# Kernel tuning notes

Measured on AMD Instinct MI355X. Metric: run time of the kernel, lower is better.

Reference implementation:

```python
import jax, jax.numpy as jnp
import numpy as np

A = 9               # anchors per location (3 scales x 3 ratios)
STRIDE = 32         # backbone stride 16 * conv1 stride 2
PRE_NMS = 2000      # boxes kept before NMS
POST_NMS = 300      # rois kept after NMS
NMS_THRESH = 0.7
MIN_SIZE = 16.0
NEG = jnp.float32(-1e30)


def _generate_anchors(base_size=16, ratios=(0.5, 1.0, 2.0), scales=(8, 16, 32)):
    xc = yc = 0.5 * (base_size - 1)
    size = float(base_size * base_size)
    anchors = []
    for r in ratios:
        ws = np.round(np.sqrt(size / r))
        hs = np.round(ws * r)
        for s in scales:
            w, h = ws * s, hs * s
            anchors.append([xc - 0.5 * (w - 1), yc - 0.5 * (h - 1),
                            xc + 0.5 * (w - 1), yc + 0.5 * (h - 1)])
    return np.array(anchors, dtype=np.float32)  # [A,4]


def _conv(x, w, b, stride, pad):
    y = jax.lax.conv_general_dilated(
        x, w, (stride, stride), ((pad, pad), (pad, pad)),
        dimension_numbers=('NCHW', 'OIHW', 'NCHW'))
    return y + b[None, :, None, None]


def _iou_matrix(boxes):
    x1, y1, x2, y2 = boxes[:, 0], boxes[:, 1], boxes[:, 2], boxes[:, 3]
    area = (x2 - x1 + 1.0) * (y2 - y1 + 1.0)
    iw = jnp.maximum(0.0, jnp.minimum(x2[:, None], x2[None, :]) - jnp.maximum(x1[:, None], x1[None, :]) + 1.0)
    ih = jnp.maximum(0.0, jnp.minimum(y2[:, None], y2[None, :]) - jnp.maximum(y1[:, None], y1[None, :]) + 1.0)
    inter = iw * ih
    return inter / (area[:, None] + area[None, :] - inter)


def _nms_single(boxes, scores):
    # boxes [K,4] sorted by score desc; scores [K] (NEG = filtered out)
    K = boxes.shape[0]
    iou = _iou_matrix(boxes)
    prio = jnp.arange(K, 0, -1)

    def step(valid, _):
        any_valid = jnp.any(valid)
        pick = jnp.argmax(jnp.where(valid, prio, 0))
        new_valid = valid & (iou[pick] <= NMS_THRESH)
        return new_valid, (pick, any_valid)

    valid0 = scores > NEG * 0.5
    _, (picks, flags) = jax.lax.scan(step, valid0, None, length=POST_NMS)
    sel = boxes[picks] * flags[:, None].astype(boxes.dtype)
    return sel, jnp.sum(flags.astype(jnp.int32))


def _proposal(deltas, scores):
    B, _, H, W = deltas.shape
    im_h, im_w = float(H * STRIDE), float(W * STRIDE)
    anchors = jnp.asarray(_generate_anchors())  # [A,4]
    sx = (jnp.arange(W) * STRIDE).astype(jnp.float32)
    sy = (jnp.arange(H) * STRIDE).astype(jnp.float32)
    gx, gy = jnp.meshgrid(sx, sy)  # [H,W] each
    shift = jnp.stack([gx, gy, gx, gy], axis=-1)  # [H,W,4]
    anc = (shift[:, :, None, :] + anchors[None, None, :, :]).reshape(-1, 4)  # [H*W*A,4]

    d = deltas.reshape(B, A, 4, H, W).transpose(0, 3, 4, 1, 2).reshape(B, -1, 4)  # [B,N,4]
    s = scores[:, A:].transpose(0, 2, 3, 1).reshape(B, -1)  # fg scores [B,N]

    ws = anc[:, 2] - anc[:, 0] + 1.0
    hs = anc[:, 3] - anc[:, 1] + 1.0
    cx = anc[:, 0] + 0.5 * ws
    cy = anc[:, 1] + 0.5 * hs
    pcx = d[:, :, 0] * ws + cx
    pcy = d[:, :, 1] * hs + cy
    pw = jnp.exp(d[:, :, 2]) * ws
    ph = jnp.exp(d[:, :, 3]) * hs
    boxes = jnp.stack([pcx - 0.5 * pw, pcy - 0.5 * ph,
                       pcx + 0.5 * pw, pcy + 0.5 * ph], axis=-1)  # [B,N,4]
    lim = jnp.array([im_w - 1, im_h - 1, im_w - 1, im_h - 1], jnp.float32)
    boxes = jnp.minimum(jnp.maximum(boxes, 0.0), lim)

    bw = boxes[..., 2] - boxes[..., 0] + 1.0
    bh = boxes[..., 3] - boxes[..., 1] + 1.0
    s = jnp.where((bw >= MIN_SIZE) & (bh >= MIN_SIZE), s, NEG)

    top_s, idx = jax.lax.top_k(s, PRE_NMS)  # sorted desc
    top_b = jnp.take_along_axis(boxes, idx[:, :, None], axis=1)  # [B,PRE,4]

    sel, num = jax.vmap(_nms_single)(top_b, top_s)  # [B,POST,4], [B]
    bidx = jnp.broadcast_to(jnp.arange(B, dtype=sel.dtype)[:, None, None], (B, POST_NMS, 1))
    rois = jnp.concatenate([bidx, sel], axis=-1)  # [B,POST,5]
    return rois, num


def setup_inputs() -> dict:
    key = jax.random.key(0)
    k = jax.random.split(key, 4)
    x = jax.random.normal(k[0], (4, 512, 96, 160), jnp.float32)
    w1 = jax.random.normal(k[1], (512, 512, 3, 3), jnp.float32) * 0.02
    b1 = jnp.zeros((512,), jnp.float32)
    w_bbox = jax.random.normal(k[2], (36, 512, 1, 1), jnp.float32) * 0.02
    b_bbox = jnp.zeros((36,), jnp.float32)
    w_cls = jax.random.normal(k[3], (18, 512, 3, 3), jnp.float32) * 0.02
    b_cls = jnp.zeros((18,), jnp.float32)
    return dict(x=x, w1=w1, b1=b1, w_bbox=w_bbox, b_bbox=b_bbox, w_cls=w_cls, b_cls=b_cls)


def reference(x, w1, b1, w_bbox, b_bbox, w_cls, b_cls):
    feat = _conv(x, w1, b1, 2, 1)           # [B,512,H/2,W/2]
    deltas = _conv(feat, w_bbox, b_bbox, 1, 0)  # [B,36,h,w]
    cls = _conv(feat, w_cls, b_cls, 1, 1)       # [B,18,h,w]
    return _proposal(deltas, cls)
```

## Files before the change

kernel.cpp:

```cpp
#include <hip/hip_runtime.h>
#include <stdint.h>

typedef unsigned long long u64;
typedef unsigned int u32;

__constant__ float c_aw[9] = {184.f,368.f,736.f,128.f,256.f,512.f, 88.f,176.f,352.f};
__constant__ float c_ah[9] = { 96.f,192.f,384.f,128.f,256.f,512.f,176.f,352.f,704.f};

__global__ __launch_bounds__(256) void transpose_k(const float* __restrict__ w1,
                                                   float* __restrict__ wt2) {
  int e = blockIdx.x * 256 + threadIdx.x;
  int m = e & 7;
  int t = e >> 3;
  int k = t % 9;
  int r = t / 9;
  int ci = r & 511;
  int g = r >> 9;
  wt2[e] = w1[(size_t)(g * 8 + m) * 4608 + ci * 9 + k];
}

__global__ __launch_bounds__(256, 3) void conv1_k(const float* __restrict__ x,
                                                  const float* __restrict__ wt2,
                                                  const float* __restrict__ b1,
                                                  float* __restrict__ feat) {
  __shared__ float xs[8 * 9 * 164];
  const int tid = threadIdx.x;
  const int lane = tid & 63;
  const int wv = __builtin_amdgcn_readfirstlane(tid >> 6);
  const int owg = lane & 15;
  const int ohl = lane >> 4;
  const int n = blockIdx.z;
  const int gg = blockIdx.x * 4 + wv;
  const int oh0 = blockIdx.y * 4;
  const int ih_base = 2 * oh0 - 1;

  int soff[6], loff[6];
  float okf[6];
  bool act[6];
#pragma unroll
  for (int it = 0; it < 6; ++it) {
    int e2 = tid + 256 * it;
    act[it] = (e2 < 1449);
    int e = act[it] ? e2 : 0;
    int ih = e / 161;
    int c = e - ih * 161;
    int gih = ih_base + ih;
    int giw = c - 1;
    bool ok = act[it] && ((unsigned)gih < 96u) && ((unsigned)giw < 160u);
    soff[it] = min(max(gih, 0), 95) * 160 + min(max(giw, 0), 159);
    loff[it] = ih * 164 + c;
    okf[it] = ok ? 1.f : 0.f;
  }

  float acc[8][5];
#pragma unroll
  for (int m = 0; m < 8; ++m)
#pragma unroll
    for (int j = 0; j < 5; ++j) acc[m][j] = 0.f;

  const float* xb = x + (size_t)n * 512 * 96 * 160;
  const float* wgb = wt2 + (size_t)gg * 512 * 72;

  float r[6][8];
#pragma unroll
  for (int it = 0; it < 6; ++it)
#pragma unroll
    for (int ci = 0; ci < 8; ++ci)
      r[it][ci] = xb[(size_t)ci * 15360 + soff[it]];

  for (int c0 = 0; c0 < 512; c0 += 8) {
    __syncthreads();
#pragma unroll
    for (int it = 0; it < 6; ++it) {
      if (act[it]) {
        const float m_ = okf[it];
#pragma unroll
        for (int ci = 0; ci < 8; ++ci)
          xs[loff[it] + ci * 1476] = m_ * r[it][ci];
      }
    }
    __syncthreads();
    if (c0 + 8 < 512) {
      const float* xn = xb + (size_t)(c0 + 8) * 15360;
#pragma unroll
      for (int it = 0; it < 6; ++it)
#pragma unroll
        for (int ci = 0; ci < 8; ++ci)
          r[it][ci] = xn[(size_t)ci * 15360 + soff[it]];
    }

    for (int ci = 0; ci < 8; ++ci) {
      const float* wp = wgb + (size_t)(c0 + ci) * 72;
      const float* xrow = &xs[(ci * 9 + 2 * ohl) * 164 + owg * 10];
#pragma unroll
      for (int kh = 0; kh < 3; ++kh) {
        float xv[12];
        const float* xr = xrow + kh * 164;
#pragma unroll
        for (int t2 = 0; t2 < 6; ++t2) {
          float2 tt = *(const float2*)(xr + 2 * t2);
          xv[2 * t2] = tt.x; xv[2 * t2 + 1] = tt.y;
        }
#pragma unroll
        for (int kw = 0; kw < 3; ++kw) {
          const float* wk = wp + (kh * 3 + kw) * 8;
#pragma unroll
          for (int j = 0; j < 5; ++j) {
            const float xj = xv[kw + 2 * j];
            acc[0][j] += wk[0] * xj; acc[1][j] += wk[1] * xj;
            acc[2][j] += wk[2] * xj; acc[3][j] += wk[3] * xj;
            acc[4][j] += wk[4] * xj; acc[5][j] += wk[5] * xj;
            acc[6][j] += wk[6] * xj; acc[7][j] += wk[7] * xj;
          }
        }
      }
    }
  }
  const int oh = oh0 + ohl;
  const int owb = owg * 5;
#pragma unroll
  for (int m = 0; m < 8; ++m) {
    const int co = gg * 8 + m;
    const float bv = b1[co];
    float* op = &feat[(((size_t)n * 512 + co) * 48 + oh) * 80 + owb];
#pragma unroll
    for (int j = 0; j < 5; ++j) op[j] = acc[m][j] + bv;
  }
}

__global__ __launch_bounds__(256) void heads_k(const float* __restrict__ feat,
                                               const float* __restrict__ wb,
                                               const float* __restrict__ bb,
                                               const float* __restrict__ wcg,
                                               const float* __restrict__ bc,
                                               float* __restrict__ deltas,
                                               float* __restrict__ s) {
  __shared__ float smem[5328];
  const int tid = threadIdx.x;

  if (blockIdx.x < 120) {
    float* fs  = smem;
    float* wsb = smem + 2048;
    const int blk = blockIdx.x;
    const int b = blk / 30;
    const int pos0 = (blk % 30) * 128;
    const int pl = tid >> 1, cg = tid & 1;
    const int cbase = cg * 18;
    float acc[18];
#pragma unroll
    for (int j = 0; j < 18; ++j) acc[j] = 0.f;
    const float* fb = feat + (size_t)b * 512 * 3840;

    for (int c0 = 0; c0 < 512; c0 += 16) {
      for (int e = tid; e < 16 * 128; e += 256)
        fs[e] = fb[(size_t)(c0 + (e >> 7)) * 3840 + pos0 + (e & 127)];
      for (int e = tid; e < 16 * 36; e += 256) {
        int ci = e / 36, c = e - ci * 36;
        wsb[e] = wb[(size_t)c * 512 + c0 + ci];
      }
      __syncthreads();
      for (int ci = 0; ci < 16; ++ci) {
        float xv = fs[ci * 128 + pl];
#pragma unroll
        for (int j = 0; j < 18; ++j) acc[j] += xv * wsb[ci * 36 + cbase + j];
      }
      __syncthreads();
    }
    size_t o = ((size_t)b * 3840 + pos0 + pl) * 36 + cbase;
#pragma unroll
    for (int j = 0; j < 18; ++j) deltas[o + j] = acc[j] + bb[cbase + j];
  } else {
    float (*fs)[3][84] = (float(*)[3][84])smem;
    float (*wc)[9][9]  = (float(*)[9][9])(smem + 4032);
    const int bid2 = blockIdx.x - 120;
    const int oh = bid2 % 48;
    const int b = bid2 / 48;
    const int pos = tid % 80;
    const int cg = tid / 80;
    float acc[3] = {0.f, 0.f, 0.f};
    const float* fb = feat + (size_t)b * 512 * 3840;

    for (int c0 = 0; c0 < 512; c0 += 16) {
      for (int e = tid; e < 16 * 246; e += 256) {
        int ci = e / 246;
        int r = e - ci * 246;
        int ihl = r / 82;
        int iw = r - ihl * 82 - 1;
        int gih = oh - 1 + ihl;
        float v = 0.f;
        if ((unsigned)gih < 48u && (unsigned)iw < 80u)
          v = fb[(size_t)(c0 + ci) * 3840 + gih * 80 + iw];
        fs[ci][ihl][iw + 1] = v;
      }
      for (int e = tid; e < 16 * 81; e += 256) {
        int ci = e / 81;
        int r = e - ci * 81;
        int co = r / 9;
        int k = r - co * 9;
        wc[ci][co][k] = wcg[((size_t)(9 + co) * 512 + c0 + ci) * 9 + k];
      }
      __syncthreads();
      if (cg < 3) {
        const int cb = cg * 3;
        for (int ci = 0; ci < 16; ++ci) {
#pragma unroll
          for (int kh = 0; kh < 3; ++kh) {
#pragma unroll
            for (int kw = 0; kw < 3; ++kw) {
              float xv = fs[ci][kh][pos + kw];
              acc[0] += xv * wc[ci][cb + 0][kh * 3 + kw];
              acc[1] += xv * wc[ci][cb + 1][kh * 3 + kw];
              acc[2] += xv * wc[ci][cb + 2][kh * 3 + kw];
            }
          }
        }
      }
      __syncthreads();
    }
    if (cg < 3) {
      const int cb = cg * 3;
      size_t o = (size_t)b * 34560 + ((size_t)oh * 80 + pos) * 9 + cb;
#pragma unroll
      for (int j = 0; j < 3; ++j) s[o + j] = acc[j] + bc[9 + cb + j];
    }
  }
}

__global__ __launch_bounds__(256) void decode_k(const float* __restrict__ deltas,
                                                const float* __restrict__ s,
                                                float* __restrict__ boxes,
                                                u64* __restrict__ keys) {
  const int g = blockIdx.x * 256 + threadIdx.x;
  const int b = g / 34560;
  const int i = g - b * 34560;
  const int pos = i / 9;
  const int a = i - pos * 9;
  const int h = pos / 80;
  const int w = pos - h * 80;
  const float gx = (float)(w * 32);
  const float gy = (float)(h * 32);
  const float aw = c_aw[a], ah = c_ah[a];
  const float x1a = 7.5f - 0.5f * (aw - 1.f);
  const float y1a = 7.5f - 0.5f * (ah - 1.f);
  const float ws_ = aw, hs_ = ah;
  const float cx = (gx + x1a) + 0.5f * ws_;
  const float cy = (gy + y1a) + 0.5f * hs_;

  const float* dp = &deltas[((size_t)b * 3840 + pos) * 36 + a * 4];
  const float d0 = dp[0], d1 = dp[1], d2 = dp[2], d3 = dp[3];
  const float pcx = __fadd_rn(__fmul_rn(d0, ws_), cx);
  const float pcy = __fadd_rn(__fmul_rn(d1, hs_), cy);
  const float pw = __fmul_rn(expf(d2), ws_);
  const float ph = __fmul_rn(expf(d3), hs_);
  float bx1 = __fsub_rn(pcx, __fmul_rn(0.5f, pw));
  float by1 = __fsub_rn(pcy, __fmul_rn(0.5f, ph));
  float bx2 = __fadd_rn(pcx, __fmul_rn(0.5f, pw));
  float by2 = __fadd_rn(pcy, __fmul_rn(0.5f, ph));
  bx1 = fminf(fmaxf(bx1, 0.f), 2559.f);
  by1 = fminf(fmaxf(by1, 0.f), 1535.f);
  bx2 = fminf(fmaxf(bx2, 0.f), 2559.f);
  by2 = fminf(fmaxf(by2, 0.f), 1535.f);
  const float bw = __fadd_rn(__fsub_rn(bx2, bx1), 1.f);
  const float bh = __fadd_rn(__fsub_rn(by2, by1), 1.f);
  float sc = s[g];
  if (!(bw >= 16.f && bh >= 16.f)) sc = -1e30f;

  float4 bo;
  bo.x = bx1; bo.y = by1; bo.z = bx2; bo.w = by2;
  *(float4*)&boxes[(size_t)g * 4] = bo;

  u32 sb = __float_as_uint(sc);
  u32 ou = (sb & 0x80000000u) ? ~sb : (sb | 0x80000000u);
  keys[g] = ((u64)ou << 32) | (u32)(~(u32)i);
}

__global__ __launch_bounds__(1024) void selcomp_k(const u64* __restrict__ keys,
                                                  u64* __restrict__ sel) {
  __shared__ u32 h[16384];
  __shared__ u64 cand[6144];
  __shared__ u32 wsum[16], wsuf[16];
  __shared__ int s_bin, s_above, s_main, s_nc;
  const int b = blockIdx.x;
  const int tid = threadIdx.x;
  const int lane = tid & 63;
  const int wv = tid >> 6;
  const u64* kb = keys + (size_t)b * 34560;

#pragma unroll
  for (int q = 0; q < 16; ++q) h[tid + 1024 * q] = 0;
  __syncthreads();
  for (int i = tid; i < 34560; i += 1024)
    atomicAdd(&h[(u32)(kb[i] >> 50)], 1u);
  __syncthreads();

  const int i0 = tid * 16;
  u32 myb[16];
  u32 tsum = 0;
#pragma unroll
  for (int q = 0; q < 16; ++q) { myb[q] = h[i0 + q]; tsum += myb[q]; }
  u32 sfx = tsum;
#pragma unroll
  for (int off = 1; off < 64; off <<= 1) {
    u32 o = __shfl_down(sfx, off, 64);
    if (lane + off < 64) sfx += o;
  }
  if (lane == 0) wsum[wv] = sfx;
  __syncthreads();
  if (tid < 16) {
    u32 v = wsum[tid];
#pragma unroll
    for (int off = 1; off < 16; off <<= 1) {
      u32 o = __shfl_down(v, off, 64);
      if (tid + off < 16) v += o;
    }
    wsuf[tid] = v;
  }
  __syncthreads();
  const u32 wave_base = (wv < 15) ? wsuf[wv + 1] : 0u;
  u32 accu = wave_base + (sfx - tsum);
#pragma unroll
  for (int q = 15; q >= 0; --q) { accu += myb[q]; h[i0 + q] = accu; }
  __syncthreads();

#pragma unroll
  for (int q = 0; q < 16; ++q) {
    int bn = i0 + q;
    u32 Si = h[bn];
    u32 Sn = (bn < 16383) ? h[bn + 1] : 0u;
    if ((int)Si >= 2000 && (int)Sn < 2000) { s_bin = bn; s_above = (int)Sn; }
  }
  if (tid == 0) { s_main = 0; s_nc = 0; }
  __syncthreads();
  const u32 B = (u32)s_bin;
  const int above = s_above;
  const int need = 2000 - above;

  for (int i = tid; i < 34560; i += 1024) {
    u64 k = kb[i];
    u32 t14 = (u32)(k >> 50);
    if (t14 > B) {
      int p = atomicAdd(&s_main, 1);
      sel[(size_t)b * 2048 + p] = k;
    } else if (t14 == B) {
      int p = atomicAdd(&s_nc, 1);
      if (p < 6144) cand[p] = k;
    }
  }
  __syncthreads();
  const int nc = min(s_nc, 6144);
  for (int c = tid; c < nc; c += 1024) {
    u64 kc = cand[c];
    int rnk = 0;
    for (int j = 0; j < nc; ++j) rnk += (cand[j] > kc) ? 1 : 0;
    if (rnk < need) sel[(size_t)b * 2048 + above + rnk] = kc;
  }
}

__global__ __launch_bounds__(1024) void sort_k(const u64* __restrict__ sel,
                                               const float* __restrict__ boxes,
                                               float* __restrict__ sx1, float* __restrict__ sy1,
                                               float* __restrict__ sx2, float* __restrict__ sy2,
                                               float* __restrict__ sar, u32* __restrict__ sval) {
  __shared__ u64 K[2048];
  __shared__ unsigned char val[2048];
  const int b = blockIdx.x;
  const int tid = threadIdx.x;

  for (int i = tid; i < 2048; i += 1024)
    K[i] = (i < 2000) ? sel[(size_t)b * 2048 + i] : 0ull;
  __syncthreads();
  for (int k2 = 2; k2 <= 2048; k2 <<= 1) {
    for (int j = k2 >> 1; j > 0; j >>= 1) {
      for (int i = tid; i < 2048; i += 1024) {
        int l = i ^ j;
        if (l > i) {
          u64 a = K[i], c = K[l];
          bool up = ((i & k2) == 0);
          if (up ? (a < c) : (a > c)) { K[i] = c; K[l] = a; }
        }
      }
      __syncthreads();
    }
  }
  for (int i = tid; i < 2048; i += 1024) {
    float x1v = 0.f, y1v = 0.f, x2v = 0.f, y2v = 0.f, arv = 1.f;
    unsigned char vb = 0;
    if (i < 2000) {
      u64 key = K[i];
      u32 ou = (u32)(key >> 32);
      int idx = (int)(~(u32)key);
      u32 sb = (ou & 0x80000000u) ? (ou & 0x7FFFFFFFu) : ~ou;
      float sc = __uint_as_float(sb);
      const float4 bo = *(const float4*)&boxes[((size_t)b * 34560 + idx) * 4];
      x1v = bo.x; y1v = bo.y; x2v = bo.z; y2v = bo.w;
      arv = __fmul_rn(__fadd_rn(__fsub_rn(bo.z, bo.x), 1.f),
                      __fadd_rn(__fsub_rn(bo.w, bo.y), 1.f));
      vb = (sc > -5e29f) ? 1 : 0;
    }
    size_t o = (size_t)b * 2048 + i;
    sx1[o] = x1v; sy1[o] = y1v; sx2[o] = x2v; sy2[o] = y2v; sar[o] = arv;
    val[i] = vb;
  }
  __syncthreads();
  if (tid < 64) {
    u32 w = 0;
#pragma unroll
    for (int q = 0; q < 32; ++q)
      w |= (val[tid * 32 + q] ? 1u : 0u) << q;
    sval[b * 64 + tid] = w;
  }
}

__global__ __launch_bounds__(256) void iou_k(const float* __restrict__ sx1, const float* __restrict__ sy1,
                                             const float* __restrict__ sx2, const float* __restrict__ sy2,
                                             const float* __restrict__ sar,
                                             u64* __restrict__ supp) {
  __shared__ float lx1[2048], ly1[2048], lx2[2048], ly2[2048], lar[2048];
  const int b = blockIdx.y;
  const int r0 = blockIdx.x * 128;
  const int tid = threadIdx.x;
  const int lane = tid & 63;
  const int wq = tid >> 6;
  const size_t base = (size_t)b * 2048;

  for (int i = tid; i < 2048; i += 256) {
    lx1[i] = sx1[base + i]; ly1[i] = sy1[base + i];
    lx2[i] = sx2[base + i]; ly2[i] = sy2[base + i];
    lar[i] = sar[base + i];
  }
  __syncthreads();

  for (int i = r0; i < r0 + 128; ++i) {
    const float px1 = lx1[i], py1 = ly1[i], px2 = lx2[i], py2 = ly2[i], pa = lar[i];
    u64* row = supp + ((size_t)b * 2048 + i) * 32;
#pragma unroll
    for (int s2 = 0; s2 < 8; ++s2) {
      const int j = s2 * 256 + wq * 64 + lane;
      float iw = __fadd_rn(__fsub_rn(fminf(px2, lx2[j]), fmaxf(px1, lx1[j])), 1.f);
      iw = fmaxf(0.f, iw);
      float ih = __fadd_rn(__fsub_rn(fminf(py2, ly2[j]), fmaxf(py1, ly1[j])), 1.f);
      ih = fmaxf(0.f, ih);
      const float inter = __fmul_rn(iw, ih);
      const float denom = __fsub_rn(__fadd_rn(pa, lar[j]), inter);
      const float iou = __fdiv_rn(inter, denom);
      const u64 bits = __ballot(iou > 0.7f);
      if (lane == 0) row[s2 * 4 + wq] = bits;
    }
  }
}

__global__ __launch_bounds__(64) void scan_k(const u32* __restrict__ sval,
                                             const u64* __restrict__ supp,
                                             const float* __restrict__ sx1, const float* __restrict__ sy1,
                                             const float* __restrict__ sx2, const float* __restrict__ sy2,
                                             float* __restrict__ out) {
  const int b = blockIdx.x;
  const int lane = threadIdx.x;
  u32 v = sval[b * 64 + lane];
  const size_t base = (size_t)b * 2048;

  int cnt = 0;
  for (int t = 0; t < 300; ++t) {
    u64 m = __ballot(v != 0);
    if (m == 0) break;
    const int f = __ffsll(m) - 1;
    const u32 fw = __shfl(v, f, 64);
    const int p = f * 32 + (__ffs(fw) - 1);
    if (lane == 0) {
      float* row = out + ((size_t)b * 300 + t) * 5;
      row[0] = (float)b;
      row[1] = sx1[base + p]; row[2] = sy1[base + p];
      row[3] = sx2[base + p]; row[4] = sy2[base + p];
    }
    cnt = t + 1;
    const u64 w8 = supp[(base + p) * 32 + (lane >> 1)];
    const u32 sup = (lane & 1) ? (u32)(w8 >> 32) : (u32)w8;
    v &= ~sup;
  }
  for (int t2 = cnt + lane; t2 < 300; t2 += 64) {
    float* row = out + ((size_t)b * 300 + t2) * 5;
    row[0] = (float)b; row[1] = 0.f; row[2] = 0.f; row[3] = 0.f; row[4] = 0.f;
  }
  if (lane == 0) out[6000 + b] = (float)cnt;
}

extern "C" void kernel_launch(void* const* d_in, const int* in_sizes, int n_in,
                              void* d_out, int out_size, void* d_ws, size_t ws_size,
                              hipStream_t stream) {
  const float* x  = (const float*)d_in[0];
  const float* w1 = (const float*)d_in[1];
  const float* b1 = (const float*)d_in[2];
  const float* wb = (const float*)d_in[3];
  const float* bb = (const float*)d_in[4];
  const float* wc = (const float*)d_in[5];
  const float* bc = (const float*)d_in[6];
  float* out = (float*)d_out;
  char* ws = (char*)d_ws;

  float* feat   = (float*)(ws + 0);
  float* wt2    = (float*)(ws + 31457280);
  float* deltas = (float*)(ws + 40894464);
  float* s      = (float*)(ws + 43106304);
  float* boxes  = (float*)(ws + 43659264);
  u64*   keys   = (u64*)  (ws + 45871104);
  u64*   sel    = (u64*)  (ws + 46977088);
  float* sx1    = (float*)(ws + 47042624);
  float* sy1    = (float*)(ws + 47075392);
  float* sx2    = (float*)(ws + 47108160);
  float* sy2    = (float*)(ws + 47140928);
  float* sar    = (float*)(ws + 47173696);
  u32*   sval   = (u32*)  (ws + 47206464);
  u64*   supp   = (u64*)  (ws + 47207488);

  hipLaunchKernelGGL(transpose_k, dim3(9216), dim3(256), 0, stream, w1, wt2);
  hipLaunchKernelGGL(conv1_k, dim3(16, 12, 4), dim3(256), 0, stream, x, wt2, b1, feat);
  hipLaunchKernelGGL(heads_k, dim3(312), dim3(256), 0, stream, feat, wb, bb, wc, bc, deltas, s);
  hipLaunchKernelGGL(decode_k, dim3(540), dim3(256), 0, stream, deltas, s, boxes, keys);
  hipLaunchKernelGGL(selcomp_k, dim3(4), dim3(1024), 0, stream, keys, sel);
  hipLaunchKernelGGL(sort_k, dim3(4), dim3(1024), 0, stream, sel, boxes, sx1, sy1, sx2, sy2, sar, sval);
  hipLaunchKernelGGL(iou_k, dim3(16, 4), dim3(256), 0, stream, sx1, sy1, sx2, sy2, sar, supp);
  hipLaunchKernelGGL(scan_k, dim3(4), dim3(64), 0, stream, sval, supp, sx1, sy1, sx2, sy2, out);
}
```

Before: 1.544 ms.

## Pack conv1 FMAs into v2f and register-prefetch tiles in head kernels

The conv1 accumulators become float2 vectors so pairs of output channels share a packed FMA (v_pk_fma_f32 on CDNA), which halves the FMA instruction count in the hot inner loop. Both branches of the heads kernel switch from direct global-to-LDS staging to a register prefetch: the next 16-channel tile is loaded into registers while the current tile is computed, and one barrier per iteration is removed. This raises register pressure and depends on the compiler actually emitting the packed instructions.

Result: faster. 1.378 ms (-10.7%).

```diff
diff --git a/kernel.cpp b/kernel.cpp
--- a/kernel.cpp
+++ b/kernel.cpp
@@ -3,6 +3,7 @@
 
 typedef unsigned long long u64;
 typedef unsigned int u32;
+typedef float v2f __attribute__((ext_vector_type(2)));
 
 __constant__ float c_aw[9] = {184.f,368.f,736.f,128.f,256.f,512.f, 88.f,176.f,352.f};
 __constant__ float c_ah[9] = { 96.f,192.f,384.f,128.f,256.f,512.f,176.f,352.f,704.f};
@@ -52,11 +53,11 @@
     okf[it] = ok ? 1.f : 0.f;
   }
 
-  float acc[8][5];
-#pragma unroll
-  for (int m = 0; m < 8; ++m)
-#pragma unroll
-    for (int j = 0; j < 5; ++j) acc[m][j] = 0.f;
+  v2f acc[4][5];
+#pragma unroll
+  for (int q = 0; q < 4; ++q)
+#pragma unroll
+    for (int j = 0; j < 5; ++j) acc[q][j] = (v2f){0.f, 0.f};
 
   const float* xb = x + (size_t)n * 512 * 96 * 160;
   const float* wgb = wt2 + (size_t)gg * 512 * 72;
@@ -103,14 +104,16 @@
         }
 #pragma unroll
         for (int kw = 0; kw < 3; ++kw) {
-          const float* wk = wp + (kh * 3 + kw) * 8;
+          const v2f* wk2 = (const v2f*)(wp + (kh * 3 + kw) * 8);
+          const v2f w0 = wk2[0], w1 = wk2[1], w2 = wk2[2], w3 = wk2[3];
 #pragma unroll
           for (int j = 0; j < 5; ++j) {
             const float xj = xv[kw + 2 * j];
-            acc[0][j] += wk[0] * xj; acc[1][j] += wk[1] * xj;
-            acc[2][j] += wk[2] * xj; acc[3][j] += wk[3] * xj;
-            acc[4][j] += wk[4] * xj; acc[5][j] += wk[5] * xj;
-            acc[6][j] += wk[6] * xj; acc[7][j] += wk[7] * xj;
+            const v2f xx = {xj, xj};
+            acc[0][j] = __builtin_elementwise_fma(w0, xx, acc[0][j]);
+            acc[1][j] = __builtin_elementwise_fma(w1, xx, acc[1][j]);
+            acc[2][j] = __builtin_elementwise_fma(w2, xx, acc[2][j]);
+            acc[3][j] = __builtin_elementwise_fma(w3, xx, acc[3][j]);
           }
         }
       }
@@ -119,12 +122,16 @@
   const int oh = oh0 + ohl;
   const int owb = owg * 5;
 #pragma unroll
-  for (int m = 0; m < 8; ++m) {
-    const int co = gg * 8 + m;
-    const float bv = b1[co];
-    float* op = &feat[(((size_t)n * 512 + co) * 48 + oh) * 80 + owb];
-#pragma unroll
-    for (int j = 0; j < 5; ++j) op[j] = acc[m][j] + bv;
+  for (int q = 0; q < 4; ++q) {
+    const int co = gg * 8 + 2 * q;
+    const float bx = b1[co], by = b1[co + 1];
+    float* opx = &feat[(((size_t)n * 512 + co) * 48 + oh) * 80 + owb];
+    float* opy = opx + 3840;
+#pragma unroll
+    for (int j = 0; j < 5; ++j) {
+      opx[j] = acc[q][j].x + bx;
+      opy[j] = acc[q][j].y + by;
+    }
   }
 }
 
@@ -146,60 +153,122 @@
     const int pos0 = (blk % 30) * 128;
     const int pl = tid >> 1, cg = tid & 1;
     const int cbase = cg * 18;
+    const float* fb = feat + (size_t)b * 512 * 3840;
+
+    int fso[8];
+#pragma unroll
+    for (int p = 0; p < 8; ++p) {
+      int e = tid + 256 * p;
+      fso[p] = (e >> 7) * 3840 + pos0 + (e & 127);
+    }
+    int wso[3]; bool wact[3];
+#pragma unroll
+    for (int p = 0; p < 3; ++p) {
+      int e = tid + 256 * p;
+      wact[p] = (e < 576);
+      int ee = wact[p] ? e : 0;
+      wso[p] = (ee % 36) * 512 + (ee / 36);
+    }
     float acc[18];
 #pragma unroll
     for (int j = 0; j < 18; ++j) acc[j] = 0.f;
-    const float* fb = feat + (size_t)b * 512 * 3840;
-
-    for (int c0 = 0; c0 < 512; c0 += 16) {
-      for (int e = tid; e < 16 * 128; e += 256)
-        fs[e] = fb[(size_t)(c0 + (e >> 7)) * 3840 + pos0 + (e & 127)];
-      for (int e = tid; e < 16 * 36; e += 256) {
-        int ci = e / 36, c = e - ci * 36;
-        wsb[e] = wb[(size_t)c * 512 + c0 + ci];
-      }
+
+    float rf[8], rw[3];
+#pragma unroll
+    for (int p = 0; p < 8; ++p) rf[p] = fb[fso[p]];
+#pragma unroll
+    for (int p = 0; p < 3; ++p) rw[p] = wb[wso[p]];
+
+    for (int t = 0; t < 32; ++t) {
       __syncthreads();
+#pragma unroll
+      for (int p = 0; p < 8; ++p) fs[tid + 256 * p] = rf[p];
+#pragma unroll
+      for (int p = 0; p < 3; ++p)
+        if (wact[p]) wsb[tid + 256 * p] = rw[p];
+      __syncthreads();
+      if (t < 31) {
+        const float* fn = fb + (size_t)(t + 1) * 16 * 3840;
+        const float* wn = wb + (t + 1) * 16;
+#pragma unroll
+        for (int p = 0; p < 8; ++p) rf[p] = fn[fso[p]];
+#pragma unroll
+        for (int p = 0; p < 3; ++p) rw[p] = wn[wso[p]];
+      }
       for (int ci = 0; ci < 16; ++ci) {
         float xv = fs[ci * 128 + pl];
 #pragma unroll
         for (int j = 0; j < 18; ++j) acc[j] += xv * wsb[ci * 36 + cbase + j];
       }
-      __syncthreads();
     }
     size_t o = ((size_t)b * 3840 + pos0 + pl) * 36 + cbase;
 #pragma unroll
     for (int j = 0; j < 18; ++j) deltas[o + j] = acc[j] + bb[cbase + j];
   } else {
-    float (*fs)[3][84] = (float(*)[3][84])smem;
-    float (*wc)[9][9]  = (float(*)[9][9])(smem + 4032);
+    float* fsf = smem;
+    float* wcf = smem + 4032;
     const int bid2 = blockIdx.x - 120;
     const int oh = bid2 % 48;
     const int b = bid2 / 48;
     const int pos = tid % 80;
     const int cg = tid / 80;
+    const float* fb = feat + (size_t)b * 512 * 3840;
+
+    int fso3[16], lof3[16];
+    float fok3[16];
+    bool fact3[16];
+#pragma unroll
+    for (int p = 0; p < 16; ++p) {
+      int e = tid + 256 * p;
+      fact3[p] = (e < 3936);
+      int ee = fact3[p] ? e : 0;
+      int ci = ee / 246;
+      int r = ee - ci * 246;
+      int ihl = r / 82;
+      int iw = r - ihl * 82 - 1;
+      int gih = oh - 1 + ihl;
+      bool ok = fact3[p] && ((unsigned)gih < 48u) && ((unsigned)iw < 80u);
+      fso3[p] = ci * 3840 + min(max(gih, 0), 47) * 80 + min(max(iw, 0), 79);
+      lof3[p] = ci * 252 + ihl * 84 + iw + 1;
+      fok3[p] = ok ? 1.f : 0.f;
+    }
+    int wso3[6]; bool wact3[6];
+#pragma unroll
+    for (int p = 0; p < 6; ++p) {
+      int e = tid + 256 * p;
+      wact3[p] = (e < 1296);
+      int ee = wact3[p] ? e : 0;
+      int ci = ee / 81;
+      int r = ee - ci * 81;
+      int co = r / 9;
+      int k = r - co * 9;
+      wso3[p] = ((size_t)(9 + co) * 512 + ci) * 9 + k;
+    }
     float acc[3] = {0.f, 0.f, 0.f};
-    const float* fb = feat + (size_t)b * 512 * 3840;
-
-    for (int c0 = 0; c0 < 512; c0 += 16) {
-      for (int e = tid; e < 16 * 246; e += 256) {
-        int ci = e / 246;
-        int r = e - ci * 246;
-        int ihl = r / 82;
-        int iw = r - ihl * 82 - 1;
-        int gih = oh - 1 + ihl;
-        float v = 0.f;
-        if ((unsigned)gih < 48u && (unsigned)iw < 80u)
-          v = fb[(size_t)(c0 + ci) * 3840 + gih * 80 + iw];
-        fs[ci][ihl][iw + 1] = v;
-      }
-      for (int e = tid; e < 16 * 81; e += 256) {
-        int ci = e / 81;
-        int r = e - ci * 81;
-        int co = r / 9;
-        int k = r - co * 9;
-        wc[ci][co][k] = wcg[((size_t)(9 + co) * 512 + c0 + ci) * 9 + k];
-      }
+
+    float rf3[16], rw3[6];
+#pragma unroll
+    for (int p = 0; p < 16; ++p) rf3[p] = fb[fso3[p]];
+#pragma unroll
+    for (int p = 0; p < 6; ++p) rw3[p] = wcg[wso3[p]];
+
+    for (int t = 0; t < 32; ++t) {
       __syncthreads();
+#pragma unroll
+      for (int p = 0; p < 16; ++p)
+        if (fact3[p]) fsf[lof3[p]] = fok3[p] * rf3[p];
+#pragma unroll
+      for (int p = 0; p < 6; ++p)
+        if (wact3[p]) wcf[tid + 256 * p] = rw3[p];
+      __syncthreads();
+      if (t < 31) {
+        const float* fn = fb + (size_t)(t + 1) * 16 * 3840;
+        const float* wn = wcg + (t + 1) * 144;
+#pragma unroll
+        for (int p = 0; p < 16; ++p) rf3[p] = fn[fso3[p]];
+#pragma unroll
+        for (int p = 0; p < 6; ++p) rw3[p] = wn[wso3[p]];
+      }
       if (cg < 3) {
         const int cb = cg * 3;
         for (int ci = 0; ci < 16; ++ci) {
@@ -207,15 +276,14 @@
           for (int kh = 0; kh < 3; ++kh) {
 #pragma unroll
             for (int kw = 0; kw < 3; ++kw) {
-              float xv = fs[ci][kh][pos + kw];
-              acc[0] += xv * wc[ci][cb + 0][kh * 3 + kw];
-              acc[1] += xv * wc[ci][cb + 1][kh * 3 + kw];
-              acc[2] += xv * wc[ci][cb + 2][kh * 3 + kw];
+              float xv = fsf[ci * 252 + kh * 84 + pos + kw];
+              acc[0] += xv * wcf[ci * 81 + (cb + 0) * 9 + kh * 3 + kw];
+              acc[1] += xv * wcf[ci * 81 + (cb + 1) * 9 + kh * 3 + kw];
+              acc[2] += xv * wcf[ci * 81 + (cb + 2) * 9 + kh * 3 + kw];
             }
           }
         }
       }
-      __syncthreads();
     }
     if (cg < 3) {
       const int cb = cg * 3;
```
